# Performance work log

Hardware: AMD Instinct MI355X
Metric: run time of the kernel (lower is better)

The kernel has to match this reference:

```python
import jax, jax.numpy as jnp
import numpy as np

GRID = 32  # hard-coded voxel resolution in the original module


def setup_inputs() -> dict:
    key = jax.random.key(0)
    k1, k2 = jax.random.split(key)
    points = jax.random.normal(k1, (4, 100000, 3), dtype=jnp.float32)
    features = jax.random.normal(k2, (4, 100000, 64), dtype=jnp.float32)
    return {"points": points, "features": features}


def reference(points, features):
    # points: [B, N, 3], features: [B, N, F]
    B, N, _ = points.shape
    Fdim = features.shape[-1]
    # Global (over whole tensor) min/max normalization, exactly as original
    pmin = points.min()
    pmax = points.max()
    normed = (points - pmin) / (pmax - pmin + 1e-6)  # in [0, 1)
    # torch: (normed // (1/32)).long() == floor(normed * 32)
    vox = jnp.floor(normed * GRID).astype(jnp.int32)  # [B, N, 3], values in [0, 31]
    gidx = vox[..., 0] * (GRID * GRID) + vox[..., 1] * GRID + vox[..., 2]  # [B, N]
    # Scatter-max into a zero-initialized grid (zeros init == implicit max with 0,
    # matching the original torch.zeros output_grid).
    grid = jnp.zeros((B, GRID ** 3, Fdim), dtype=features.dtype)
    batch_ids = jnp.arange(B, dtype=jnp.int32)[:, None]  # [B, 1] broadcast over N
    grid = grid.at[batch_ids, gidx].max(features)
    return grid.reshape(B, GRID, GRID, GRID, Fdim)
```

## Files before the change

### kernel.cpp

```cpp
#include <hip/hip_runtime.h>

#define GRID3 32768
#define FDIM 64
#define CHUNK 512
#define GBLOCKS 2048

__device__ __forceinline__ unsigned int enc_f32(float f) {
    unsigned int u = __float_as_uint(f);
    return (u & 0x80000000u) ? ~u : (u | 0x80000000u);
}
__device__ __forceinline__ float dec_f32(unsigned int u) {
    u = (u & 0x80000000u) ? (u ^ 0x80000000u) : ~u;
    return __uint_as_float(u);
}

__device__ __forceinline__ int bin_of(float x, float y, float z,
                                      float pmin, float denom) {
    int vx = (int)(((x - pmin) / denom) * 32.0f);
    int vy = (int)(((y - pmin) / denom) * 32.0f);
    int vz = (int)(((z - pmin) / denom) * 32.0f);
    vx = min(max(vx, 0), 31);
    vy = min(max(vy, 0), 31);
    vz = min(max(vz, 0), 31);
    return (vx << 10) + (vy << 5) + vz;
}

__global__ void init_ws_kernel(unsigned int* ws) {
    ws[0] = 0xFFFFFFFFu;
    ws[1] = 0u;
    ws[2] = 0u;
}

__global__ void minmax_kernel(const float* __restrict__ pts, int n,
                              unsigned int* __restrict__ ws) {
    float lmin = INFINITY, lmax = -INFINITY;
    const float4* p4 = reinterpret_cast<const float4*>(pts);
    const int n4 = n >> 2;
    for (int i = blockIdx.x * blockDim.x + threadIdx.x; i < n4;
         i += gridDim.x * blockDim.x) {
        float4 v = p4[i];
        lmin = fminf(lmin, fminf(fminf(v.x, v.y), fminf(v.z, v.w)));
        lmax = fmaxf(lmax, fmaxf(fmaxf(v.x, v.y), fmaxf(v.z, v.w)));
    }
    for (int i = (n4 << 2) + blockIdx.x * blockDim.x + threadIdx.x; i < n;
         i += gridDim.x * blockDim.x) {
        float v = pts[i];
        lmin = fminf(lmin, v);
        lmax = fmaxf(lmax, v);
    }
    __shared__ float smin[256], smax[256];
    smin[threadIdx.x] = lmin;
    smax[threadIdx.x] = lmax;
    __syncthreads();
    for (int s = 128; s > 0; s >>= 1) {
        if (threadIdx.x < (unsigned)s) {
            smin[threadIdx.x] = fminf(smin[threadIdx.x], smin[threadIdx.x + s]);
            smax[threadIdx.x] = fmaxf(smax[threadIdx.x], smax[threadIdx.x + s]);
        }
        __syncthreads();
    }
    if (threadIdx.x == 0) {
        atomicMin(&ws[0], enc_f32(smin[0]));
        atomicMax(&ws[1], enc_f32(smax[0]));
    }
}

__global__ void count_kernel(const float* __restrict__ pts,
                             const unsigned int* __restrict__ ws,
                             unsigned int* __restrict__ cnt,
                             int ntot, int N) {
    int i = blockIdx.x * blockDim.x + threadIdx.x;
    if (i >= ntot) return;
    float pmin = dec_f32(ws[0]);
    float denom = dec_f32(ws[1]) - pmin + 1e-6f;
    int bin = (i / N) * GRID3 +
              bin_of(pts[i * 3], pts[i * 3 + 1], pts[i * 3 + 2], pmin, denom);
    atomicAdd(&cnt[bin], 1u);
}

__global__ void compact_kernel(const unsigned int* __restrict__ cnt,
                               unsigned int* __restrict__ occ,
                               unsigned int* __restrict__ noccp, int nbins) {
    int i = blockIdx.x * blockDim.x + threadIdx.x;
    if (i >= nbins) return;
    if (cnt[i] != 0u) {
        unsigned int pos = atomicAdd(noccp, 1u);
        occ[pos] = (unsigned int)i;
    }
}

__global__ __launch_bounds__(256)
void scanA_kernel(const unsigned int* __restrict__ cnt,
                  unsigned int* __restrict__ bsum, int nbins) {
    __shared__ unsigned int s[256];
    int base = blockIdx.x * CHUNK;
    int t = threadIdx.x;
    unsigned int a = (base + t < nbins) ? cnt[base + t] : 0u;
    unsigned int b = (base + t + 256 < nbins) ? cnt[base + t + 256] : 0u;
    s[t] = a + b;
    __syncthreads();
    for (int st = 128; st > 0; st >>= 1) {
        if (t < st) s[t] += s[t + st];
        __syncthreads();
    }
    if (t == 0) bsum[blockIdx.x] = s[0];
}

__global__ __launch_bounds__(1024)
void scanB_kernel(unsigned int* __restrict__ bsum, int nchunks) {
    __shared__ unsigned int s[1024];
    int t = threadIdx.x;
    unsigned int own = (t < nchunks) ? bsum[t] : 0u;
    s[t] = own;
    __syncthreads();
    for (int off = 1; off < 1024; off <<= 1) {
        unsigned int v = (t >= off) ? s[t - off] : 0u;
        __syncthreads();
        s[t] += v;
        __syncthreads();
    }
    if (t < nchunks) bsum[t] = s[t] - own;
}

__global__ __launch_bounds__(256)
void scanC_kernel(unsigned int* __restrict__ cnt,
                  const unsigned int* __restrict__ bsum, int nbins) {
    __shared__ unsigned int s[256];
    int t = threadIdx.x;
    int base = blockIdx.x * CHUNK;
    int i0 = base + 2 * t;
    unsigned int a = (i0 < nbins) ? cnt[i0] : 0u;
    unsigned int b = (i0 + 1 < nbins) ? cnt[i0 + 1] : 0u;
    unsigned int p = a + b;
    s[t] = p;
    __syncthreads();
    for (int off = 1; off < 256; off <<= 1) {
        unsigned int v = (t >= off) ? s[t - off] : 0u;
        __syncthreads();
        s[t] += v;
        __syncthreads();
    }
    unsigned int excl = s[t] - p + bsum[blockIdx.x];
    if (i0 < nbins) cnt[i0] = excl;
    if (i0 + 1 < nbins) cnt[i0 + 1] = excl + a;
}

__global__ void fill_kernel(const float* __restrict__ pts,
                            const unsigned int* __restrict__ ws,
                            unsigned int* __restrict__ cursor,
                            unsigned int* __restrict__ idx,
                            int ntot, int N) {
    int i = blockIdx.x * blockDim.x + threadIdx.x;
    if (i >= ntot) return;
    float pmin = dec_f32(ws[0]);
    float denom = dec_f32(ws[1]) - pmin + 1e-6f;
    int bin = (i / N) * GRID3 +
              bin_of(pts[i * 3], pts[i * 3 + 1], pts[i * 3 + 2], pmin, denom);
    unsigned int pos = atomicAdd(&cursor[bin], 1u);
    idx[pos] = (unsigned int)i;
}

__global__ __launch_bounds__(256)
void gatherocc_kernel(const float* __restrict__ feat,
                      const unsigned int* __restrict__ cursor,
                      const unsigned int* __restrict__ idx,
                      const unsigned int* __restrict__ occ,
                      const unsigned int* __restrict__ noccp,
                      float* __restrict__ out) {
    int wid = blockIdx.x * 4 + (threadIdx.x >> 6);
    int lane = threadIdx.x & 63;
    int nocc = (int)*noccp;
    const int nwaves = GBLOCKS * 4;
    const float* fl = feat + lane;

    for (int w = wid; w < nocc; w += nwaves) {
        int bin = (int)occ[w];
        unsigned int s = bin ? cursor[bin - 1] : 0u;
        unsigned int e = cursor[bin];
        float acc = 0.0f;
        unsigned int k = s;
        for (; k + 16 <= e; k += 16) {
            unsigned int p[16];
#pragma unroll
            for (int j = 0; j < 16; ++j) p[j] = idx[k + j];
            float f[16];
#pragma unroll
            for (int j = 0; j < 16; ++j) f[j] = fl[(size_t)p[j] * FDIM];
            float m = f[0];
#pragma unroll
            for (int j = 1; j < 16; ++j) m = fmaxf(m, f[j]);
            acc = fmaxf(acc, m);
        }
        for (; k < e; ++k)
            acc = fmaxf(acc, fl[(size_t)idx[k] * FDIM]);
        out[(size_t)bin * FDIM + lane] = acc;
    }
}

__global__ __launch_bounds__(256)
void gather_kernel(const float* __restrict__ feat,
                   const unsigned int* __restrict__ cursor,
                   const unsigned int* __restrict__ idx,
                   float* __restrict__ out, int nbins) {
    int bin = blockIdx.x * 4 + (threadIdx.x >> 6);
    int lane = threadIdx.x & 63;
    if (bin >= nbins) return;
    unsigned int s = bin ? cursor[bin - 1] : 0u;
    unsigned int e = cursor[bin];
    const float* fl = feat + lane;
    float acc = 0.0f;
    unsigned int k = s;
    for (; k + 16 <= e; k += 16) {
        unsigned int p[16];
#pragma unroll
        for (int j = 0; j < 16; ++j) p[j] = idx[k + j];
        float f[16];
#pragma unroll
        for (int j = 0; j < 16; ++j) f[j] = fl[(size_t)p[j] * FDIM];
        float m = f[0];
#pragma unroll
        for (int j = 1; j < 16; ++j) m = fmaxf(m, f[j]);
        acc = fmaxf(acc, m);
    }
    for (; k < e; ++k)
        acc = fmaxf(acc, fl[(size_t)idx[k] * FDIM]);
    out[(size_t)bin * FDIM + lane] = acc;
}

__global__ void scatter_kernel(const float* __restrict__ pts,
                               const float* __restrict__ feat,
                               const unsigned int* __restrict__ ws,
                               unsigned int* __restrict__ out,
                               int ntot, int N) {
    int lane = threadIdx.x & 63;
    int p = blockIdx.x * 4 + (threadIdx.x >> 6);
    if (p >= ntot) return;
    float pmin = dec_f32(ws[0]);
    float denom = dec_f32(ws[1]) - pmin + 1e-6f;
    int gidx = bin_of(pts[p * 3], pts[p * 3 + 1], pts[p * 3 + 2], pmin, denom);
    int b = p / N;
    float f = feat[(size_t)p * FDIM + lane];
    if (f > 0.0f) {
        unsigned int* addr = out + ((size_t)b * GRID3 + gidx) * FDIM + lane;
        atomicMax(addr, __float_as_uint(f));
    }
}

extern "C" void kernel_launch(void* const* d_in, const int* in_sizes, int n_in,
                              void* d_out, int out_size, void* d_ws, size_t ws_size,
                              hipStream_t stream) {
    const float* pts = (const float*)d_in[0];
    const float* feat = (const float*)d_in[1];
    unsigned int* ws = (unsigned int*)d_ws;

    int npts3 = in_sizes[0];
    int ntot = npts3 / 3;
    int B = out_size / (GRID3 * FDIM);
    int N = ntot / B;
    int nbins = B * GRID3;
    int nchunks = (nbins + CHUNK - 1) / CHUNK;

    unsigned int* bsum = ws + 64;
    unsigned int* cursor = bsum + 1024;
    unsigned int* idx = cursor + nbins;
    unsigned int* occ = idx + ntot;
    size_t need_occ = (size_t)(64 + 1024 + 2 * (size_t)nbins + ntot) * 4;
    size_t need_csr = (size_t)(64 + 1024 + nbins + (size_t)ntot) * 4;

    hipLaunchKernelGGL(init_ws_kernel, dim3(1), dim3(1), 0, stream, ws);
    hipLaunchKernelGGL(minmax_kernel, dim3(512), dim3(256), 0, stream,
                       pts, npts3, ws);

    int pblocks = (ntot + 255) / 256;
    if (ws_size >= need_occ && nchunks <= 1024) {
        hipMemsetAsync(cursor, 0, (size_t)nbins * 4, stream);
        hipLaunchKernelGGL(count_kernel, dim3(pblocks), dim3(256), 0, stream,
                           pts, ws, cursor, ntot, N);
        hipLaunchKernelGGL(compact_kernel, dim3((nbins + 255) / 256), dim3(256),
                           0, stream, cursor, occ, &ws[2], nbins);
        hipLaunchKernelGGL(scanA_kernel, dim3(nchunks), dim3(256), 0, stream,
                           cursor, bsum, nbins);
        hipLaunchKernelGGL(scanB_kernel, dim3(1), dim3(1024), 0, stream,
                           bsum, nchunks);
        hipLaunchKernelGGL(scanC_kernel, dim3(nchunks), dim3(256), 0, stream,
                           cursor, bsum, nbins);
        hipLaunchKernelGGL(fill_kernel, dim3(pblocks), dim3(256), 0, stream,
                           pts, ws, cursor, idx, ntot, N);
        hipMemsetAsync(d_out, 0, (size_t)out_size * sizeof(float), stream);
        hipLaunchKernelGGL(gatherocc_kernel, dim3(GBLOCKS), dim3(256), 0,
                           stream, feat, cursor, idx, occ, &ws[2],
                           (float*)d_out);
    } else if (ws_size >= need_csr && nchunks <= 1024) {
        hipMemsetAsync(cursor, 0, (size_t)nbins * 4, stream);
        hipLaunchKernelGGL(count_kernel, dim3(pblocks), dim3(256), 0, stream,
                           pts, ws, cursor, ntot, N);
        hipLaunchKernelGGL(scanA_kernel, dim3(nchunks), dim3(256), 0, stream,
                           cursor, bsum, nbins);
        hipLaunchKernelGGL(scanB_kernel, dim3(1), dim3(1024), 0, stream,
                           bsum, nchunks);
        hipLaunchKernelGGL(scanC_kernel, dim3(nchunks), dim3(256), 0, stream,
                           cursor, bsum, nbins);
        hipLaunchKernelGGL(fill_kernel, dim3(pblocks), dim3(256), 0, stream,
                           pts, ws, cursor, idx, ntot, N);
        hipLaunchKernelGGL(gather_kernel, dim3((nbins + 3) / 4), dim3(256), 0,
                           stream, feat, cursor, idx, (float*)d_out, nbins);
    } else {
        hipMemsetAsync(d_out, 0, (size_t)out_size * sizeof(float), stream);
        hipLaunchKernelGGL(scatter_kernel, dim3((ntot + 3) / 4), dim3(256), 0,
                           stream, pts, feat, ws, (unsigned int*)d_out, ntot, N);
    }
}
```

Before: 292.0 us.

## Compact occupied bins with precomputed ranges and launch one wave per bin

The occupied-bin compaction now runs after the fill pass and stores (bin, start, end) as a uint4, so the gather wave no longer reads cursor entries to find its range. The gather kernel drops the grid-stride loop over 2048 blocks and launches one wave per possible bin, with waves beyond the occupied count exiting early. The remainder loop becomes clamped 16-wide loads that re-read the last index, and the max reduction is written as a tree. This trades more launched (mostly empty) blocks and redundant loads on tail iterations for fewer dependent loads and better latency hiding per bin.

```diff
diff --git a/kernel.cpp b/kernel.cpp
--- a/kernel.cpp
+++ b/kernel.cpp
@@ -3,7 +3,6 @@
 #define GRID3 32768
 #define FDIM 64
 #define CHUNK 512
-#define GBLOCKS 2048
 
 __device__ __forceinline__ unsigned int enc_f32(float f) {
     unsigned int u = __float_as_uint(f);
@@ -76,17 +75,6 @@
     int bin = (i / N) * GRID3 +
               bin_of(pts[i * 3], pts[i * 3 + 1], pts[i * 3 + 2], pmin, denom);
     atomicAdd(&cnt[bin], 1u);
-}
-
-__global__ void compact_kernel(const unsigned int* __restrict__ cnt,
-                               unsigned int* __restrict__ occ,
-                               unsigned int* __restrict__ noccp, int nbins) {
-    int i = blockIdx.x * blockDim.x + threadIdx.x;
-    if (i >= nbins) return;
-    if (cnt[i] != 0u) {
-        unsigned int pos = atomicAdd(noccp, 1u);
-        occ[pos] = (unsigned int)i;
-    }
 }
 
 __global__ __launch_bounds__(256)
@@ -160,41 +148,53 @@
     idx[pos] = (unsigned int)i;
 }
 
+__global__ void compact2_kernel(const unsigned int* __restrict__ cursor,
+                                uint4* __restrict__ occ4,
+                                unsigned int* __restrict__ noccp, int nbins) {
+    int i = blockIdx.x * blockDim.x + threadIdx.x;
+    if (i >= nbins) return;
+    unsigned int s = i ? cursor[i - 1] : 0u;
+    unsigned int e = cursor[i];
+    if (e != s) {
+        unsigned int pos = atomicAdd(noccp, 1u);
+        occ4[pos] = make_uint4((unsigned int)i, s, e, 0u);
+    }
+}
+
 __global__ __launch_bounds__(256)
-void gatherocc_kernel(const float* __restrict__ feat,
-                      const unsigned int* __restrict__ cursor,
+void gatherbin_kernel(const float* __restrict__ feat,
+                      const uint4* __restrict__ occ4,
+                      const unsigned int* __restrict__ noccp,
                       const unsigned int* __restrict__ idx,
-                      const unsigned int* __restrict__ occ,
-                      const unsigned int* __restrict__ noccp,
                       float* __restrict__ out) {
     int wid = blockIdx.x * 4 + (threadIdx.x >> 6);
     int lane = threadIdx.x & 63;
-    int nocc = (int)*noccp;
-    const int nwaves = GBLOCKS * 4;
+    unsigned int nocc = *noccp;
+    if ((unsigned int)wid >= nocc) return;
+
+    uint4 o = occ4[wid];
+    unsigned int bin = o.x, s = o.y, e = o.z;
     const float* fl = feat + lane;
 
-    for (int w = wid; w < nocc; w += nwaves) {
-        int bin = (int)occ[w];
-        unsigned int s = bin ? cursor[bin - 1] : 0u;
-        unsigned int e = cursor[bin];
-        float acc = 0.0f;
-        unsigned int k = s;
-        for (; k + 16 <= e; k += 16) {
-            unsigned int p[16];
-#pragma unroll
-            for (int j = 0; j < 16; ++j) p[j] = idx[k + j];
-            float f[16];
-#pragma unroll
-            for (int j = 0; j < 16; ++j) f[j] = fl[(size_t)p[j] * FDIM];
-            float m = f[0];
-#pragma unroll
-            for (int j = 1; j < 16; ++j) m = fmaxf(m, f[j]);
-            acc = fmaxf(acc, m);
-        }
-        for (; k < e; ++k)
-            acc = fmaxf(acc, fl[(size_t)idx[k] * FDIM]);
-        out[(size_t)bin * FDIM + lane] = acc;
-    }
+    float acc = 0.0f;
+    for (unsigned int k = s; k < e; k += 16) {
+        unsigned int p[16];
+#pragma unroll
+        for (int j = 0; j < 16; ++j)
+            p[j] = idx[min(k + (unsigned int)j, e - 1u)];
+        float f[16];
+#pragma unroll
+        for (int j = 0; j < 16; ++j)
+            f[j] = fl[(size_t)p[j] * FDIM];
+        float m01 = fmaxf(f[0], f[1]),  m23 = fmaxf(f[2], f[3]);
+        float m45 = fmaxf(f[4], f[5]),  m67 = fmaxf(f[6], f[7]);
+        float m89 = fmaxf(f[8], f[9]),  mab = fmaxf(f[10], f[11]);
+        float mcd = fmaxf(f[12], f[13]), mef = fmaxf(f[14], f[15]);
+        float a0 = fmaxf(fmaxf(m01, m23), fmaxf(m45, m67));
+        float a1 = fmaxf(fmaxf(m89, mab), fmaxf(mcd, mef));
+        acc = fmaxf(acc, fmaxf(a0, a1));
+    }
+    out[(size_t)bin * FDIM + lane] = acc;
 }
 
 __global__ __launch_bounds__(256)
@@ -263,8 +263,9 @@
     unsigned int* bsum = ws + 64;
     unsigned int* cursor = bsum + 1024;
     unsigned int* idx = cursor + nbins;
-    unsigned int* occ = idx + ntot;
-    size_t need_occ = (size_t)(64 + 1024 + 2 * (size_t)nbins + ntot) * 4;
+    size_t occ_off = ((size_t)(64 + 1024 + nbins + ntot) + 3) & ~(size_t)3;
+    uint4* occ4 = (uint4*)(ws + occ_off);
+    size_t need_occ = (occ_off + 4 * (size_t)nbins) * 4;
     size_t need_csr = (size_t)(64 + 1024 + nbins + (size_t)ntot) * 4;
 
     hipLaunchKernelGGL(init_ws_kernel, dim3(1), dim3(1), 0, stream, ws);
@@ -276,8 +277,6 @@
         hipMemsetAsync(cursor, 0, (size_t)nbins * 4, stream);
         hipLaunchKernelGGL(count_kernel, dim3(pblocks), dim3(256), 0, stream,
                            pts, ws, cursor, ntot, N);
-        hipLaunchKernelGGL(compact_kernel, dim3((nbins + 255) / 256), dim3(256),
-                           0, stream, cursor, occ, &ws[2], nbins);
         hipLaunchKernelGGL(scanA_kernel, dim3(nchunks), dim3(256), 0, stream,
                            cursor, bsum, nbins);
         hipLaunchKernelGGL(scanB_kernel, dim3(1), dim3(1024), 0, stream,
@@ -286,10 +285,11 @@
                            cursor, bsum, nbins);
         hipLaunchKernelGGL(fill_kernel, dim3(pblocks), dim3(256), 0, stream,
                            pts, ws, cursor, idx, ntot, N);
+        hipLaunchKernelGGL(compact2_kernel, dim3((nbins + 255) / 256),
+                           dim3(256), 0, stream, cursor, occ4, &ws[2], nbins);
         hipMemsetAsync(d_out, 0, (size_t)out_size * sizeof(float), stream);
-        hipLaunchKernelGGL(gatherocc_kernel, dim3(GBLOCKS), dim3(256), 0,
-                           stream, feat, cursor, idx, occ, &ws[2],
-                           (float*)d_out);
+        hipLaunchKernelGGL(gatherbin_kernel, dim3((nbins + 3) / 4), dim3(256),
+                           0, stream, feat, occ4, &ws[2], idx, (float*)d_out);
     } else if (ws_size >= need_csr && nchunks <= 1024) {
         hipMemsetAsync(cursor, 0, (size_t)nbins * 4, stream);
         hipLaunchKernelGGL(count_kernel, dim3(pblocks), dim3(256), 0, stream,
```

After: 279.3 us. 1.05x faster.
